# Performance work log

Measured on AMD Instinct MI355X. Metric: run time of the kernel, lower is better.

The kernel has to match this reference:

```python
import jax, jax.numpy as jnp
import numpy as np

D_MODEL = 768
D_FF = 3072
N_HEADS = 12
HEAD_DIM = D_MODEL // N_HEADS
SUB_SCALE = 0.5
LN_EPS = 1e-5


def _layer_norm(x, g, b):
    mu = jnp.mean(x, axis=-1, keepdims=True)
    var = jnp.var(x, axis=-1, keepdims=True)
    return (x - mu) * jax.lax.rsqrt(var + LN_EPS) * g + b


def setup_inputs() -> dict:
    key = jax.random.key(0)
    ks = jax.random.split(key, 12)
    B, T = 1, 4096
    s = lambda fan_in: 1.0 / np.sqrt(fan_in)
    return {
        "x": jax.random.normal(ks[0], (B, T, D_MODEL), dtype=jnp.float32),
        "ln1_g": jnp.ones((D_MODEL,), jnp.float32),
        "ln1_b": jnp.zeros((D_MODEL,), jnp.float32),
        "ln2_g": jnp.ones((D_MODEL,), jnp.float32),
        "ln2_b": jnp.zeros((D_MODEL,), jnp.float32),
        "qkv_w": jax.random.normal(ks[1], (D_MODEL, 3 * D_MODEL), jnp.float32) * s(D_MODEL),
        "qkv_b": jnp.zeros((3 * D_MODEL,), jnp.float32),
        "out_w": jax.random.normal(ks[2], (D_MODEL, D_MODEL), jnp.float32) * s(D_MODEL),
        "out_b": jnp.zeros((D_MODEL,), jnp.float32),
        "fc1_w": jax.random.normal(ks[3], (D_MODEL, D_FF), jnp.float32) * s(D_MODEL),
        "fc1_b": jnp.zeros((D_FF,), jnp.float32),
        "fc2_w": jax.random.normal(ks[4], (D_FF, D_MODEL), jnp.float32) * s(D_FF),
        "fc2_b": jnp.zeros((D_MODEL,), jnp.float32),
    }


def reference(x, ln1_g, ln1_b, ln2_g, ln2_b, qkv_w, qkv_b, out_w, out_b,
              fc1_w, fc1_b, fc2_w, fc2_b):
    B, T, C = x.shape
    # --- attention sub-block ---
    h = _layer_norm(x, ln1_g, ln1_b) * SUB_SCALE
    qkv = h @ qkv_w + qkv_b                      # [B,T,3C]
    q, k, v = jnp.split(qkv, 3, axis=-1)
    split = lambda t: t.reshape(B, T, N_HEADS, HEAD_DIM).transpose(0, 2, 1, 3)
    q, k, v = split(q), split(k), split(v)       # [B,H,T,Hd]
    scores = jnp.einsum('bhqd,bhkd->bhqk', q, k) / jnp.sqrt(jnp.float32(HEAD_DIM))
    weights = jax.nn.softmax(scores, axis=-1)    # [B,H,T,T] (no mask, as in source)
    attn = jnp.einsum('bhqk,bhkd->bhqd', weights, v)
    attn = attn.transpose(0, 2, 1, 3).reshape(B, T, C)
    x = x + attn @ out_w + out_b
    # --- MLP sub-block ---
    h2 = _layer_norm(x, ln2_g, ln2_b) * SUB_SCALE
    h2 = jax.nn.gelu(h2 @ fc1_w + fc1_b, approximate=False)  # nn.GELU() = exact erf
    h2 = h2 @ fc2_w + fc2_b
    return x + h2
```

## Files before the change

### kernel.cpp

```cpp
#include <hip/hip_runtime.h>
#include <hip/hip_bf16.h>
#include <math.h>

#define TSEQ 4096
#define DMODEL 768
#define DFF 3072
#define NHEADS 12
#define HDIM 64

typedef __attribute__((ext_vector_type(8))) short short8;
typedef __attribute__((ext_vector_type(4))) float f32x4;
typedef unsigned short ushort;
typedef unsigned int uint;

typedef __attribute__((address_space(1))) ushort as1_ushort;
typedef __attribute__((address_space(3))) ushort as3_ushort;

__device__ __forceinline__ void gl_lds16(const ushort* g, const ushort* l) {
    __builtin_amdgcn_global_load_lds((as1_ushort*)(uintptr_t)g,
                                     (as3_ushort*)(uint)(uintptr_t)l, 16, 0, 0);
}

__device__ __forceinline__ ushort f2bf(float f) {
    union { float f; unsigned i; } c; c.f = f;
    unsigned x = c.i;
    unsigned r = x + 0x7FFFu + ((x >> 16) & 1u);
    return (ushort)(r >> 16);
}
__device__ __forceinline__ float asf(uint u) {
    union { unsigned i; float f; } c; c.i = u; return c.f;
}
__device__ __forceinline__ float gelu_fast(float v) {
    float y = v * (0.7978845608f + 0.03567740814f * v * v);
    float u = exp2f(y * -2.8853900817779268f);
    float r;
    asm("v_rcp_f32 %0, %1" : "=v"(r) : "v"(1.f + u));
    return v * r;
}

__global__ __launch_bounds__(256) void ln_half_kernel(
    const float* __restrict__ x, const float* __restrict__ g,
    const float* __restrict__ b, ushort* __restrict__ out)
{
    int row = blockIdx.x;
    const float* xr = x + (size_t)row * DMODEL;
    float v[3];
    float s = 0.f, s2 = 0.f;
    #pragma unroll
    for (int i = 0; i < 3; i++) {
        v[i] = xr[threadIdx.x + 256 * i];
        s += v[i]; s2 += v[i] * v[i];
    }
    #pragma unroll
    for (int m = 1; m < 64; m <<= 1) { s += __shfl_xor(s, m, 64); s2 += __shfl_xor(s2, m, 64); }
    __shared__ float ss[4], ss2[4];
    int wid = threadIdx.x >> 6;
    if ((threadIdx.x & 63) == 0) { ss[wid] = s; ss2[wid] = s2; }
    __syncthreads();
    s = ss[0] + ss[1] + ss[2] + ss[3];
    s2 = ss2[0] + ss2[1] + ss2[2] + ss2[3];
    float mu = s * (1.f / DMODEL);
    float var = s2 * (1.f / DMODEL) - mu * mu;
    float rs = rsqrtf(var + 1e-5f);
    #pragma unroll
    for (int i = 0; i < 3; i++) {
        int c = threadIdx.x + 256 * i;
        float h = (v[i] - mu) * rs * g[c] + b[c];
        out[(size_t)row * DMODEL + c] = f2bf(h * 0.5f);
    }
}

__global__ __launch_bounds__(256) void transpose_cast_kernel(
    const float* __restrict__ in, ushort* __restrict__ out, int K, int N)
{
    __shared__ float tile[32][33];
    int k0 = blockIdx.x * 32, n0 = blockIdx.y * 32;
    int c = threadIdx.x & 31, r0 = threadIdx.x >> 5;
    #pragma unroll
    for (int i = 0; i < 4; i++) {
        int r = r0 + i * 8;
        tile[r][c] = in[(size_t)(k0 + r) * N + n0 + c];
    }
    __syncthreads();
    #pragma unroll
    for (int i = 0; i < 4; i++) {
        int r = r0 + i * 8;
        out[(size_t)(n0 + r) * K + k0 + c] = f2bf(tile[c][r]);
    }
}

__global__ __launch_bounds__(256) void vtrans_kernel(
    const ushort* __restrict__ qkvb, ushort* __restrict__ vT)
{
    __shared__ ushort tile[64][72];
    int t0 = blockIdx.x * 64, d0 = blockIdx.y * 64;
    int tid = threadIdx.x;
    int r = tid >> 2, c = (tid & 3) * 16;
    const ushort* src = qkvb + (size_t)(t0 + r) * 2304 + 1536 + d0 + c;
    *(short8*)&tile[r][c]     = *(const short8*)src;
    *(short8*)&tile[r][c + 8] = *(const short8*)(src + 8);
    __syncthreads();
    int d = tid & 63, gq = tid >> 6;
    short8 w0, w1;
    #pragma unroll
    for (int i = 0; i < 8; i++) w0[i] = (short)tile[gq * 16 + i][d];
    #pragma unroll
    for (int i = 0; i < 8; i++) w1[i] = (short)tile[gq * 16 + 8 + i][d];
    ushort* dst = vT + (size_t)(d0 + d) * TSEQ + t0 + gq * 16;
    *(short8*)dst       = w0;
    *(short8*)(dst + 8) = w1;
}

template<int EPI>
__global__ __launch_bounds__(256) void gemm_kernel(
    const ushort* __restrict__ A, const ushort* __restrict__ Bt,
    const float* __restrict__ bias, const float* __restrict__ res,
    void* __restrict__ out, int M, int N, int K)
{
    __shared__ ushort As[2][128 * 32];
    __shared__ ushort Bs[2][128 * 32];
    int bm = blockIdx.x * 128, bn = blockIdx.y * 128;
    int tid = threadIdx.x;
    int wid = tid >> 6, lane = tid & 63;
    int wm = (wid >> 1) * 64, wn = (wid & 1) * 64;
    int lg = lane >> 4, lr = lane & 15;
    int srow = lane >> 2, scol = (lane & 3) * 8;
    f32x4 acc[4][4] = {};

    const ushort* ga0 = A  + (size_t)(bm + wid * 16 + srow) * K + scol;
    const ushort* ga1 = A  + (size_t)(bm + 64 + wid * 16 + srow) * K + scol;
    const ushort* gb0 = Bt + (size_t)(bn + wid * 16 + srow) * K + scol;
    const ushort* gb1 = Bt + (size_t)(bn + 64 + wid * 16 + srow) * K + scol;

    gl_lds16(ga0, &As[0][wid * 512]);
    gl_lds16(ga1, &As[0][2048 + wid * 512]);
    gl_lds16(gb0, &Bs[0][wid * 512]);
    gl_lds16(gb1, &Bs[0][2048 + wid * 512]);

    int nt = K >> 5;
    for (int t = 0; t < nt; t++) {
        int cur = t & 1;
        __syncthreads();
        if (t + 1 < nt) {
            int k0 = (t + 1) << 5;
            int nb = cur ^ 1;
            gl_lds16(ga0 + k0, &As[nb][wid * 512]);
            gl_lds16(ga1 + k0, &As[nb][2048 + wid * 512]);
            gl_lds16(gb0 + k0, &Bs[nb][wid * 512]);
            gl_lds16(gb1 + k0, &Bs[nb][2048 + wid * 512]);
        }
        short8 a[4], b[4];
        #pragma unroll
        for (int mi = 0; mi < 4; mi++) a[mi] = *(const short8*)&As[cur][(wm + mi * 16 + lr) * 32 + lg * 8];
        #pragma unroll
        for (int ni = 0; ni < 4; ni++) b[ni] = *(const short8*)&Bs[cur][(wn + ni * 16 + lr) * 32 + lg * 8];
        #pragma unroll
        for (int mi = 0; mi < 4; mi++)
            #pragma unroll
            for (int ni = 0; ni < 4; ni++)
                acc[mi][ni] = __builtin_amdgcn_mfma_f32_16x16x32_bf16(a[mi], b[ni], acc[mi][ni], 0, 0, 0);
    }

    #pragma unroll
    for (int mi = 0; mi < 4; mi++) {
        #pragma unroll
        for (int ni = 0; ni < 4; ni++) {
            int col = bn + wn + ni * 16 + lr;
            float bv = bias[col];
            #pragma unroll
            for (int r = 0; r < 4; r++) {
                int row = bm + wm + mi * 16 + lg * 4 + r;
                float v = acc[mi][ni][r] + bv;
                size_t idx = (size_t)row * N + col;
                if (EPI == 0) {
                    ((ushort*)out)[idx] = f2bf(v);
                } else if (EPI == 1) {
                    ((ushort*)out)[idx] = f2bf(gelu_fast(v));
                } else {
                    ((float*)out)[idx] = v + res[idx];
                }
            }
        }
    }
}

template<int EPI>
__global__ __launch_bounds__(256) void gemm_n64_kernel(
    const ushort* __restrict__ A, const ushort* __restrict__ Bt,
    const float* __restrict__ bias, const float* __restrict__ res,
    void* __restrict__ out, int M, int N, int K)
{
    __shared__ ushort As[2][128 * 32];
    __shared__ ushort Bs[2][64 * 32];
    int bm = blockIdx.x * 128, bn = blockIdx.y * 64;
    int tid = threadIdx.x;
    int wid = tid >> 6, lane = tid & 63;
    int wm = (wid >> 1) * 64, wn = (wid & 1) * 32;
    int lg = lane >> 4, lr = lane & 15;
    int srow = lane >> 2, scol = (lane & 3) * 8;
    f32x4 acc[4][2] = {};

    const ushort* ga0 = A  + (size_t)(bm + wid * 16 + srow) * K + scol;
    const ushort* ga1 = A  + (size_t)(bm + 64 + wid * 16 + srow) * K + scol;
    const ushort* gb0 = Bt + (size_t)(bn + wid * 16 + srow) * K + scol;

    gl_lds16(ga0, &As[0][wid * 512]);
    gl_lds16(ga1, &As[0][2048 + wid * 512]);
    gl_lds16(gb0, &Bs[0][wid * 512]);

    int nt = K >> 5;
    for (int t = 0; t < nt; t++) {
        int cur = t & 1;
        __syncthreads();
        if (t + 1 < nt) {
            int k0 = (t + 1) << 5;
            int nb = cur ^ 1;
            gl_lds16(ga0 + k0, &As[nb][wid * 512]);
            gl_lds16(ga1 + k0, &As[nb][2048 + wid * 512]);
            gl_lds16(gb0 + k0, &Bs[nb][wid * 512]);
        }
        short8 a[4], b[2];
        #pragma unroll
        for (int mi = 0; mi < 4; mi++) a[mi] = *(const short8*)&As[cur][(wm + mi * 16 + lr) * 32 + lg * 8];
        #pragma unroll
        for (int ni = 0; ni < 2; ni++) b[ni] = *(const short8*)&Bs[cur][(wn + ni * 16 + lr) * 32 + lg * 8];
        #pragma unroll
        for (int mi = 0; mi < 4; mi++)
            #pragma unroll
            for (int ni = 0; ni < 2; ni++)
                acc[mi][ni] = __builtin_amdgcn_mfma_f32_16x16x32_bf16(a[mi], b[ni], acc[mi][ni], 0, 0, 0);
    }

    #pragma unroll
    for (int mi = 0; mi < 4; mi++) {
        #pragma unroll
        for (int ni = 0; ni < 2; ni++) {
            int col = bn + wn + ni * 16 + lr;
            float bv = bias[col];
            #pragma unroll
            for (int r = 0; r < 4; r++) {
                int row = bm + wm + mi * 16 + lg * 4 + r;
                float v = acc[mi][ni][r] + bv;
                size_t idx = (size_t)row * N + col;
                if (EPI == 0) {
                    ((ushort*)out)[idx] = f2bf(v);
                } else if (EPI == 1) {
                    ((ushort*)out)[idx] = f2bf(gelu_fast(v));
                } else {
                    ((float*)out)[idx] = v + res[idx];
                }
            }
        }
    }
}

__global__ __launch_bounds__(512) void attn_kernel(
    const ushort* __restrict__ qkv, const ushort* __restrict__ vT,
    ushort* __restrict__ Opart, float* __restrict__ ml)
{
    int combo = blockIdx.x % 48;
    int qblk  = blockIdx.x / 48;
    int h     = combo >> 2;
    int split = combo & 3;
    __shared__ ushort smem[16384 + 256 * 40];
    ushort* Ps = smem + 16384;
    int tid = threadIdx.x, wid = tid >> 6, lane = tid & 63;
    int lg = lane >> 4, lr = lane & 15;
    const float C1 = 0.18033688011112042f;
    const float KC = 12.0f * C1;
    int x7 = lr & 7;

    {
        int row = tid >> 1;
        int u0 = (tid & 1) * 4;
        int r7 = row & 7;
        const ushort* src = qkv + (size_t)(qblk * 256 + row) * 2304 + h * HDIM;
        #pragma unroll
        for (int i = 0; i < 4; i++) {
            int u = u0 + i;
            *(short8*)&smem[row * 64 + ((u ^ r7) * 8)] = *(const short8*)(src + (size_t)(u * 8));
        }
    }
    int q0row = (wid * 32 + lr) * 64;
    int q1row = q0row + 16 * 64;
    short8 qa0 = *(const short8*)&smem[q0row + (lg ^ x7) * 8];
    short8 qa1 = *(const short8*)&smem[q0row + ((4 + lg) ^ x7) * 8];
    short8 qb0 = *(const short8*)&smem[q1row + (lg ^ x7) * 8];
    short8 qb1 = *(const short8*)&smem[q1row + ((4 + lg) ^ x7) * 8];
    __syncthreads();

    short8 vone;
    #pragma unroll
    for (int i = 0; i < 8; i++) vone[i] = (short)0x3F80;

    int krow = tid >> 3;
    int kunit = (tid & 7) ^ (krow & 7);
    const ushort* kg = qkv + (size_t)(split * 1024 + krow) * 2304 + DMODEL + h * HDIM + kunit * 8;
    const ushort* vgp = vT + (size_t)(h * HDIM + krow) * TSEQ + split * 1024 + kunit * 8;

    gl_lds16(kg, &smem[tid * 8]);
    gl_lds16(vgp, &smem[8192 + tid * 8]);
    kg += 64 * 2304;
    vgp += 64;

    f32x4 o0[4] = {}, o1[4] = {};
    f32x4 s0sum = {}, s1sum = {};
    const int NT = 16;
    int prow0 = (wid * 32 + lr) * 40;
    int prow1 = prow0 + 16 * 40;

    for (int kt = 0; kt < NT; kt++) {
        int cur = kt & 1, nb = cur ^ 1;
        __syncthreads();
        if (kt + 1 < NT) {
            gl_lds16(kg, &smem[nb * 4096 + tid * 8]);
            gl_lds16(vgp, &smem[8192 + nb * 4096 + tid * 8]);
            kg += 64 * 2304;
            vgp += 64;
        }
        const ushort* kb = &smem[cur * 4096];
        const ushort* vb = &smem[8192 + cur * 4096];

        f32x4 st0[4] = {}, st1[4] = {};
        __builtin_amdgcn_s_setprio(1);
        #pragma unroll
        for (int ki = 0; ki < 4; ki++) {
            const ushort* kr = &kb[(ki * 16 + lr) * 64];
            short8 k0 = *(const short8*)&kr[(lg ^ x7) * 8];
            short8 k1 = *(const short8*)&kr[((4 + lg) ^ x7) * 8];
            st0[ki] = __builtin_amdgcn_mfma_f32_16x16x32_bf16(k0, qa0, st0[ki], 0, 0, 0);
            st0[ki] = __builtin_amdgcn_mfma_f32_16x16x32_bf16(k1, qa1, st0[ki], 0, 0, 0);
            st1[ki] = __builtin_amdgcn_mfma_f32_16x16x32_bf16(k0, qb0, st1[ki], 0, 0, 0);
            st1[ki] = __builtin_amdgcn_mfma_f32_16x16x32_bf16(k1, qb1, st1[ki], 0, 0, 0);
        }
        __builtin_amdgcn_s_setprio(0);

        uint2 c0[4], c1[4];
        #pragma unroll
        for (int ki = 0; ki < 4; ki++) {
            #pragma unroll
            for (int r = 0; r < 4; r++) st0[ki][r] = exp2f(st0[ki][r] * C1 - KC);
            asm("v_cvt_pk_bf16_f32 %0, %1, %2" : "=v"(c0[ki].x) : "v"(st0[ki][0]), "v"(st0[ki][1]));
            asm("v_cvt_pk_bf16_f32 %0, %1, %2" : "=v"(c0[ki].y) : "v"(st0[ki][2]), "v"(st0[ki][3]));
        }
        #pragma unroll
        for (int ki = 0; ki < 4; ki++) {
            #pragma unroll
            for (int r = 0; r < 4; r++) st1[ki][r] = exp2f(st1[ki][r] * C1 - KC);
            asm("v_cvt_pk_bf16_f32 %0, %1, %2" : "=v"(c1[ki].x) : "v"(st1[ki][0]), "v"(st1[ki][1]));
            asm("v_cvt_pk_bf16_f32 %0, %1, %2" : "=v"(c1[ki].y) : "v"(st1[ki][2]), "v"(st1[ki][3]));
        }

        *(uint2*)&Ps[prow0 + lg * 4]      = c0[0];
        *(uint2*)&Ps[prow0 + 16 + lg * 4] = c0[1];
        *(uint2*)&Ps[prow1 + lg * 4]      = c1[0];
        *(uint2*)&Ps[prow1 + 16 + lg * 4] = c1[1];
        {
            short8 pa00 = *(const short8*)&Ps[prow0 + lg * 8];
            short8 pa10 = *(const short8*)&Ps[prow1 + lg * 8];
            __builtin_amdgcn_s_setprio(1);
            s0sum = __builtin_amdgcn_mfma_f32_16x16x32_bf16(pa00, vone, s0sum, 0, 0, 0);
            s1sum = __builtin_amdgcn_mfma_f32_16x16x32_bf16(pa10, vone, s1sum, 0, 0, 0);
            #pragma unroll
            for (int ni = 0; ni < 4; ni++) {
                short8 b0 = *(const short8*)&vb[(ni * 16 + lr) * 64 + (lg ^ x7) * 8];
                o0[ni] = __builtin_amdgcn_mfma_f32_16x16x32_bf16(pa00, b0, o0[ni], 0, 0, 0);
                o1[ni] = __builtin_amdgcn_mfma_f32_16x16x32_bf16(pa10, b0, o1[ni], 0, 0, 0);
            }
            __builtin_amdgcn_s_setprio(0);
        }
        *(uint2*)&Ps[prow0 + lg * 4]      = c0[2];
        *(uint2*)&Ps[prow0 + 16 + lg * 4] = c0[3];
        *(uint2*)&Ps[prow1 + lg * 4]      = c1[2];
        *(uint2*)&Ps[prow1 + 16 + lg * 4] = c1[3];
        {
            short8 pa01 = *(const short8*)&Ps[prow0 + lg * 8];
            short8 pa11 = *(const short8*)&Ps[prow1 + lg * 8];
            __builtin_amdgcn_s_setprio(1);
            s0sum = __builtin_amdgcn_mfma_f32_16x16x32_bf16(pa01, vone, s0sum, 0, 0, 0);
            s1sum = __builtin_amdgcn_mfma_f32_16x16x32_bf16(pa11, vone, s1sum, 0, 0, 0);
            #pragma unroll
            for (int ni = 0; ni < 4; ni++) {
                short8 b1 = *(const short8*)&vb[(ni * 16 + lr) * 64 + ((4 + lg) ^ x7) * 8];
                o0[ni] = __builtin_amdgcn_mfma_f32_16x16x32_bf16(pa01, b1, o0[ni], 0, 0, 0);
                o1[ni] = __builtin_amdgcn_mfma_f32_16x16x32_bf16(pa11, b1, o1[ni], 0, 0, 0);
            }
            __builtin_amdgcn_s_setprio(0);
        }
    }

    if (lr == 0) {
        #pragma unroll
        for (int r = 0; r < 4; r++) {
            int q0 = qblk * 256 + wid * 32 + lg * 4 + r;
            ml[((size_t)split * NHEADS + h) * TSEQ + q0]      = s0sum[r];
            ml[((size_t)split * NHEADS + h) * TSEQ + q0 + 16] = s1sum[r];
        }
    }
    #pragma unroll
    for (int ni = 0; ni < 4; ni++)
        #pragma unroll
        for (int r = 0; r < 4; r++) {
            int q0 = qblk * 256 + wid * 32 + lg * 4 + r;
            int dcol = ni * 16 + lr;
            Opart[((size_t)split * TSEQ + q0) * DMODEL + h * HDIM + dcol]      = f2bf(o0[ni][r]);
            Opart[((size_t)split * TSEQ + q0 + 16) * DMODEL + h * HDIM + dcol] = f2bf(o1[ni][r]);
        }
}

__global__ __launch_bounds__(256) void attn_combine_kernel(
    const ushort* __restrict__ Opart, const float* __restrict__ ml,
    ushort* __restrict__ attnb)
{
    int gid = blockIdx.x * 256 + threadIdx.x;
    int q = gid / 192;
    int c = (gid - q * 192) * 4;
    int hh = c >> 6;
    float denom = 0.f;
    float a0 = 0.f, a1 = 0.f, a2 = 0.f, a3 = 0.f;
    #pragma unroll
    for (int s = 0; s < 4; s++) {
        denom += ml[((size_t)s * NHEADS + hh) * TSEQ + q];
        uint2 ov = *(const uint2*)&Opart[((size_t)s * TSEQ + q) * DMODEL + c];
        a0 += asf(ov.x << 16);
        a1 += asf(ov.x & 0xFFFF0000u);
        a2 += asf(ov.y << 16);
        a3 += asf(ov.y & 0xFFFF0000u);
    }
    float rd = 1.f / denom;
    uint2 stv;
    stv.x = (uint)f2bf(a0 * rd) | ((uint)f2bf(a1 * rd) << 16);
    stv.y = (uint)f2bf(a2 * rd) | ((uint)f2bf(a3 * rd) << 16);
    *(uint2*)&attnb[(size_t)q * DMODEL + c] = stv;
}

extern "C" void kernel_launch(void* const* d_in, const int* in_sizes, int n_in,
                              void* d_out, int out_size, void* d_ws, size_t ws_size,
                              hipStream_t stream)
{
    const float* x      = (const float*)d_in[0];
    const float* ln1_g  = (const float*)d_in[1];
    const float* ln1_b  = (const float*)d_in[2];
    const float* ln2_g  = (const float*)d_in[3];
    const float* ln2_b  = (const float*)d_in[4];
    const float* qkv_w  = (const float*)d_in[5];
    const float* qkv_b  = (const float*)d_in[6];
    const float* out_w  = (const float*)d_in[7];
    const float* out_b  = (const float*)d_in[8];
    const float* fc1_w  = (const float*)d_in[9];
    const float* fc1_b  = (const float*)d_in[10];
    const float* fc2_w  = (const float*)d_in[11];
    const float* fc2_b  = (const float*)d_in[12];
    (void)in_sizes; (void)n_in; (void)out_size; (void)ws_size;

    char* p = (char*)d_ws;
    ushort* qkvb  = (ushort*)p;                 p += (size_t)TSEQ * DFF * 2;
    ushort* hb    = (ushort*)p;                 p += (size_t)TSEQ * DMODEL * 2;
    ushort* attnb = (ushort*)p;                 p += (size_t)TSEQ * DMODEL * 2;
    float*  x2    = (float*)p;                  p += (size_t)TSEQ * DMODEL * 4;
    ushort* qkv_wT = (ushort*)p;                p += (size_t)(3 * DMODEL) * DMODEL * 2;
    ushort* out_wT = (ushort*)p;                p += (size_t)DMODEL * DMODEL * 2;
    ushort* fc1_wT = (ushort*)p;                p += (size_t)DFF * DMODEL * 2;
    ushort* fc2_wT = (ushort*)p;                p += (size_t)DMODEL * DFF * 2;
    ushort* Opart  = (ushort*)p;                p += (size_t)4 * TSEQ * DMODEL * 2;
    float*  mlbuf  = (float*)p;                 p += (size_t)4 * NHEADS * TSEQ * 4;
    ushort* vTb    = (ushort*)p;                p += (size_t)DMODEL * TSEQ * 2;
    ushort* gb = qkvb;

    transpose_cast_kernel<<<dim3(DMODEL / 32, 3 * DMODEL / 32), 256, 0, stream>>>(qkv_w, qkv_wT, DMODEL, 3 * DMODEL);
    transpose_cast_kernel<<<dim3(DMODEL / 32, DMODEL / 32), 256, 0, stream>>>(out_w, out_wT, DMODEL, DMODEL);
    transpose_cast_kernel<<<dim3(DMODEL / 32, DFF / 32), 256, 0, stream>>>(fc1_w, fc1_wT, DMODEL, DFF);
    transpose_cast_kernel<<<dim3(DFF / 32, DMODEL / 32), 256, 0, stream>>>(fc2_w, fc2_wT, DFF, DMODEL);

    ln_half_kernel<<<TSEQ, 256, 0, stream>>>(x, ln1_g, ln1_b, hb);
    gemm_kernel<0><<<dim3(TSEQ / 128, 3 * DMODEL / 128), 256, 0, stream>>>(
        hb, qkv_wT, qkv_b, nullptr, qkvb, TSEQ, 3 * DMODEL, DMODEL);
    vtrans_kernel<<<dim3(TSEQ / 64, DMODEL / 64), 256, 0, stream>>>(qkvb, vTb);
    attn_kernel<<<dim3((TSEQ / 256) * NHEADS * 4), 512, 0, stream>>>(qkvb, vTb, Opart, mlbuf);
    attn_combine_kernel<<<(TSEQ * DMODEL / 4) / 256, 256, 0, stream>>>(Opart, mlbuf, attnb);
    gemm_n64_kernel<2><<<dim3(TSEQ / 128, DMODEL / 64), 256, 0, stream>>>(
        attnb, out_wT, out_b, x, x2, TSEQ, DMODEL, DMODEL);
    ln_half_kernel<<<TSEQ, 256, 0, stream>>>(x2, ln2_g, ln2_b, hb);
    gemm_kernel<1><<<dim3(TSEQ / 128, DFF / 128), 256, 0, stream>>>(
        hb, fc1_wT, fc1_b, nullptr, gb, TSEQ, DFF, DMODEL);
    gemm_n64_kernel<2><<<dim3(TSEQ / 128, DMODEL / 64), 256, 0, stream>>>(
        gb, fc2_wT, fc2_b, x2, (float*)d_out, TSEQ, DMODEL, DFF);
}
```

Baseline: 218.8 us.

## Fuse V transpose into QKV GEMM epilogue and retile N=768 GEMMs to 64x64

The QKV GEMM epilogue now writes the V section directly in transposed layout (packed 4 bf16 per store), which removes the separate vtrans kernel and its extra read and write of V. The out-proj and fc2 GEMMs switch from 128x64 to 64x64 tiles, which doubles the block count for better CU occupancy. They also use an XOR-swizzled LDS layout to reduce bank conflicts. The smaller tiles lower per-block data reuse, and the transposed V stores are strided 8-byte writes.

```diff
diff --git a/kernel.cpp b/kernel.cpp
--- a/kernel.cpp
+++ b/kernel.cpp
@@ -89,33 +89,11 @@
     }
 }
 
-__global__ __launch_bounds__(256) void vtrans_kernel(
-    const ushort* __restrict__ qkvb, ushort* __restrict__ vT)
-{
-    __shared__ ushort tile[64][72];
-    int t0 = blockIdx.x * 64, d0 = blockIdx.y * 64;
-    int tid = threadIdx.x;
-    int r = tid >> 2, c = (tid & 3) * 16;
-    const ushort* src = qkvb + (size_t)(t0 + r) * 2304 + 1536 + d0 + c;
-    *(short8*)&tile[r][c]     = *(const short8*)src;
-    *(short8*)&tile[r][c + 8] = *(const short8*)(src + 8);
-    __syncthreads();
-    int d = tid & 63, gq = tid >> 6;
-    short8 w0, w1;
-    #pragma unroll
-    for (int i = 0; i < 8; i++) w0[i] = (short)tile[gq * 16 + i][d];
-    #pragma unroll
-    for (int i = 0; i < 8; i++) w1[i] = (short)tile[gq * 16 + 8 + i][d];
-    ushort* dst = vT + (size_t)(d0 + d) * TSEQ + t0 + gq * 16;
-    *(short8*)dst       = w0;
-    *(short8*)(dst + 8) = w1;
-}
-
 template<int EPI>
 __global__ __launch_bounds__(256) void gemm_kernel(
     const ushort* __restrict__ A, const ushort* __restrict__ Bt,
     const float* __restrict__ bias, const float* __restrict__ res,
-    void* __restrict__ out, int M, int N, int K)
+    void* __restrict__ out, ushort* __restrict__ vTout, int M, int N, int K)
 {
     __shared__ ushort As[2][128 * 32];
     __shared__ ushort Bs[2][128 * 32];
@@ -167,17 +145,25 @@
         for (int ni = 0; ni < 4; ni++) {
             int col = bn + wn + ni * 16 + lr;
             float bv = bias[col];
-            #pragma unroll
-            for (int r = 0; r < 4; r++) {
-                int row = bm + wm + mi * 16 + lg * 4 + r;
-                float v = acc[mi][ni][r] + bv;
-                size_t idx = (size_t)row * N + col;
-                if (EPI == 0) {
-                    ((ushort*)out)[idx] = f2bf(v);
-                } else if (EPI == 1) {
-                    ((ushort*)out)[idx] = f2bf(gelu_fast(v));
-                } else {
-                    ((float*)out)[idx] = v + res[idx];
+            if (EPI == 3 && bn >= 1536) {
+                int row0 = bm + wm + mi * 16 + lg * 4;
+                uint2 pk;
+                pk.x = (uint)f2bf(acc[mi][ni][0] + bv) | ((uint)f2bf(acc[mi][ni][1] + bv) << 16);
+                pk.y = (uint)f2bf(acc[mi][ni][2] + bv) | ((uint)f2bf(acc[mi][ni][3] + bv) << 16);
+                *(uint2*)&vTout[(size_t)(col - 1536) * TSEQ + row0] = pk;
+            } else {
+                #pragma unroll
+                for (int r = 0; r < 4; r++) {
+                    int row = bm + wm + mi * 16 + lg * 4 + r;
+                    float v = acc[mi][ni][r] + bv;
+                    size_t idx = (size_t)row * N + col;
+                    if (EPI == 1) {
+                        ((ushort*)out)[idx] = f2bf(gelu_fast(v));
+                    } else if (EPI == 2) {
+                        ((float*)out)[idx] = v + res[idx];
+                    } else {
+                        ((ushort*)out)[idx] = f2bf(v);
+                    }
                 }
             }
         }
@@ -185,28 +171,27 @@
 }
 
 template<int EPI>
-__global__ __launch_bounds__(256) void gemm_n64_kernel(
+__global__ __launch_bounds__(256) void gemm_64_kernel(
     const ushort* __restrict__ A, const ushort* __restrict__ Bt,
     const float* __restrict__ bias, const float* __restrict__ res,
     void* __restrict__ out, int M, int N, int K)
 {
-    __shared__ ushort As[2][128 * 32];
+    __shared__ ushort As[2][64 * 32];
     __shared__ ushort Bs[2][64 * 32];
-    int bm = blockIdx.x * 128, bn = blockIdx.y * 64;
+    int bm = blockIdx.x * 64, bn = blockIdx.y * 64;
     int tid = threadIdx.x;
     int wid = tid >> 6, lane = tid & 63;
-    int wm = (wid >> 1) * 64, wn = (wid & 1) * 32;
+    int wm = (wid >> 1) * 32, wn = (wid & 1) * 32;
     int lg = lane >> 4, lr = lane & 15;
-    int srow = lane >> 2, scol = (lane & 3) * 8;
-    f32x4 acc[4][2] = {};
-
-    const ushort* ga0 = A  + (size_t)(bm + wid * 16 + srow) * K + scol;
-    const ushort* ga1 = A  + (size_t)(bm + 64 + wid * 16 + srow) * K + scol;
-    const ushort* gb0 = Bt + (size_t)(bn + wid * 16 + srow) * K + scol;
-
-    gl_lds16(ga0, &As[0][wid * 512]);
-    gl_lds16(ga1, &As[0][2048 + wid * 512]);
-    gl_lds16(gb0, &Bs[0][wid * 512]);
+    int srow = tid >> 2;
+    int sunit = (tid & 3) ^ (srow & 3);
+    f32x4 acc[2][2] = {};
+
+    const ushort* ga = A  + (size_t)(bm + srow) * K + sunit * 8;
+    const ushort* gb = Bt + (size_t)(bn + srow) * K + sunit * 8;
+
+    gl_lds16(ga, &As[0][tid * 8]);
+    gl_lds16(gb, &Bs[0][tid * 8]);
 
     int nt = K >> 5;
     for (int t = 0; t < nt; t++) {
@@ -215,24 +200,29 @@
         if (t + 1 < nt) {
             int k0 = (t + 1) << 5;
             int nb = cur ^ 1;
-            gl_lds16(ga0 + k0, &As[nb][wid * 512]);
-            gl_lds16(ga1 + k0, &As[nb][2048 + wid * 512]);
-            gl_lds16(gb0 + k0, &Bs[nb][wid * 512]);
-        }
-        short8 a[4], b[2];
-        #pragma unroll
-        for (int mi = 0; mi < 4; mi++) a[mi] = *(const short8*)&As[cur][(wm + mi * 16 + lr) * 32 + lg * 8];
-        #pragma unroll
-        for (int ni = 0; ni < 2; ni++) b[ni] = *(const short8*)&Bs[cur][(wn + ni * 16 + lr) * 32 + lg * 8];
-        #pragma unroll
-        for (int mi = 0; mi < 4; mi++)
+            gl_lds16(ga + k0, &As[nb][tid * 8]);
+            gl_lds16(gb + k0, &Bs[nb][tid * 8]);
+        }
+        short8 a[2], b[2];
+        #pragma unroll
+        for (int mi = 0; mi < 2; mi++) {
+            int row = wm + mi * 16 + lr;
+            a[mi] = *(const short8*)&As[cur][row * 32 + ((lg ^ (row & 3)) * 8)];
+        }
+        #pragma unroll
+        for (int ni = 0; ni < 2; ni++) {
+            int row = wn + ni * 16 + lr;
+            b[ni] = *(const short8*)&Bs[cur][row * 32 + ((lg ^ (row & 3)) * 8)];
+        }
+        #pragma unroll
+        for (int mi = 0; mi < 2; mi++)
             #pragma unroll
             for (int ni = 0; ni < 2; ni++)
                 acc[mi][ni] = __builtin_amdgcn_mfma_f32_16x16x32_bf16(a[mi], b[ni], acc[mi][ni], 0, 0, 0);
     }
 
     #pragma unroll
-    for (int mi = 0; mi < 4; mi++) {
+    for (int mi = 0; mi < 2; mi++) {
         #pragma unroll
         for (int ni = 0; ni < 2; ni++) {
             int col = bn + wn + ni * 16 + lr;
@@ -473,16 +463,15 @@
     transpose_cast_kernel<<<dim3(DFF / 32, DMODEL / 32), 256, 0, stream>>>(fc2_w, fc2_wT, DFF, DMODEL);
 
     ln_half_kernel<<<TSEQ, 256, 0, stream>>>(x, ln1_g, ln1_b, hb);
-    gemm_kernel<0><<<dim3(TSEQ / 128, 3 * DMODEL / 128), 256, 0, stream>>>(
-        hb, qkv_wT, qkv_b, nullptr, qkvb, TSEQ, 3 * DMODEL, DMODEL);
-    vtrans_kernel<<<dim3(TSEQ / 64, DMODEL / 64), 256, 0, stream>>>(qkvb, vTb);
+    gemm_kernel<3><<<dim3(TSEQ / 128, 3 * DMODEL / 128), 256, 0, stream>>>(
+        hb, qkv_wT, qkv_b, nullptr, qkvb, vTb, TSEQ, 3 * DMODEL, DMODEL);
     attn_kernel<<<dim3((TSEQ / 256) * NHEADS * 4), 512, 0, stream>>>(qkvb, vTb, Opart, mlbuf);
     attn_combine_kernel<<<(TSEQ * DMODEL / 4) / 256, 256, 0, stream>>>(Opart, mlbuf, attnb);
-    gemm_n64_kernel<2><<<dim3(TSEQ / 128, DMODEL / 64), 256, 0, stream>>>(
+    gemm_64_kernel<2><<<dim3(TSEQ / 64, DMODEL / 64), 256, 0, stream>>>(
         attnb, out_wT, out_b, x, x2, TSEQ, DMODEL, DMODEL);
     ln_half_kernel<<<TSEQ, 256, 0, stream>>>(x2, ln2_g, ln2_b, hb);
     gemm_kernel<1><<<dim3(TSEQ / 128, DFF / 128), 256, 0, stream>>>(
-        hb, fc1_wT, fc1_b, nullptr, gb, TSEQ, DFF, DMODEL);
-    gemm_n64_kernel<2><<<dim3(TSEQ / 128, DMODEL / 64), 256, 0, stream>>>(
+        hb, fc1_wT, fc1_b, nullptr, gb, nullptr, TSEQ, DFF, DMODEL);
+    gemm_64_kernel<2><<<dim3(TSEQ / 64, DMODEL / 64), 256, 0, stream>>>(
         gb, fc2_wT, fc2_b, x2, (float*)d_out, TSEQ, DMODEL, DFF);
 }
```

Result: faster. 212.2 us (-3.0%).
